# Optimization experiments

Hardware: AMD Instinct MI355X
Metric: run time of the kernel (lower is better)

## Reference

```python
import jax, jax.numpy as jnp
import numpy as np

B, C_IN, H, W = 8, 64, 224, 224
C_OUT, HID = 64, 64
KH = KW = 3
IN_SZ = C_IN * KH * KW  # 576, unfold feature size (c, kh, kw order)


def setup_inputs() -> dict:
    key = jax.random.key(0)
    k_x, k_w1, k_b1, k_w2, k_b2 = jax.random.split(key, 5)
    bound1 = 1.0 / np.sqrt(IN_SZ)
    bound2 = 1.0 / np.sqrt(HID)
    return {
        "x": jax.random.normal(k_x, (B, C_IN, H, W), dtype=jnp.float32),
        "W1": jax.random.uniform(k_w1, (HID, IN_SZ), jnp.float32, -bound1, bound1),
        "b1": jax.random.uniform(k_b1, (HID,), jnp.float32, -bound1, bound1),
        "W2": jax.random.uniform(k_w2, (C_OUT, HID), jnp.float32, -bound2, bound2),
        "b2": jax.random.uniform(k_b2, (C_OUT,), jnp.float32, -bound2, bound2),
    }


def reference(x, W1, b1, W2, b2):
    # First Linear over unfold patches == implicit-GEMM conv: W1 rows are
    # flattened (c, kh, kw) exactly matching F.unfold's feature ordering.
    w_conv = W1.reshape(HID, C_IN, KH, KW)
    h = jax.lax.conv_general_dilated(
        x, w_conv,
        window_strides=(1, 1),
        padding=((1, 1), (1, 1)),
        rhs_dilation=(1, 1),
        dimension_numbers=("NCHW", "OIHW", "NCHW"),
    ) + b1[None, :, None, None]
    h = jax.nn.relu(h)
    # Second Linear acts per patch location == pointwise (1x1) contraction.
    out = jnp.einsum("bchw,oc->bohw", h, W2) + b2[None, :, None, None]
    return out
```

## Files before the change

### kernel.cpp

```cpp
#include <hip/hip_runtime.h>

typedef __attribute__((ext_vector_type(8))) short bf16x8;
typedef __attribute__((ext_vector_type(4))) float f32x4;

static constexpr int HH = 224, WW = 224;
static constexpr int CIN = 64;

__device__ __forceinline__ ushort f2bf(float f) {
    unsigned u = __builtin_bit_cast(unsigned, f);
    u += 0x7FFFu + ((u >> 16) & 1u);
    return (ushort)(u >> 16);
}

__global__ void prep_kernel(const float* __restrict__ W1, const float* __restrict__ W2,
                            ushort* __restrict__ w1r, ushort* __restrict__ w2r) {
    const int idx = blockIdx.x * 256 + threadIdx.x;
    if (idx < 36864) {
        const int ch = idx >> 12;
        const int n = (idx >> 6) & 63;
        const int c = idx & 63;
        w1r[idx] = f2bf(W1[n * 576 + c * 9 + ch]);
    } else if (idx < 40960) {
        const int j = idx - 36864;
        w2r[j] = f2bf(W2[j]);
    }
}

__global__ __launch_bounds__(256, 3)
void mlpconv_kernel(const float* __restrict__ xin, const ushort* __restrict__ w1r,
                    const float* __restrict__ b1, const ushort* __restrict__ w2r,
                    const float* __restrict__ b2, float* __restrict__ out) {
    __shared__ ushort xs[10 * 40 * 64];

    const int tid = threadIdx.x;
    const int wave = tid >> 6;
    const int lane = tid & 63;
    const int l15 = lane & 15;
    const int quad = lane >> 4;

    const int x0 = blockIdx.x * 32;
    const int y0 = blockIdx.y * 8;
    const int b = blockIdx.z;

    const float* xg = xin + (size_t)b * (CIN * HH * WW);

    for (int e = tid; e < 6400; e += 256) {
        const int i = e % 10;
        const int t = e / 10;
        const int c = t & 63;
        const int r = t >> 6;
        const int gy = y0 + r - 1;
        const int gx4 = x0 - 4 + i * 4;
        float4 v = make_float4(0.f, 0.f, 0.f, 0.f);
        if (((unsigned)gy < (unsigned)HH) && ((unsigned)gx4 <= 220u))
            v = *reinterpret_cast<const float4*>(xg + (c * HH + gy) * WW + gx4);
        const int p0 = r * 40 + i * 4;
        xs[(p0 + 0) * 64 + (c ^ (((p0 + 0) & 7) * 8))] = f2bf(v.x);
        xs[(p0 + 1) * 64 + (c ^ (((p0 + 1) & 7) * 8))] = f2bf(v.y);
        xs[(p0 + 2) * 64 + (c ^ (((p0 + 2) & 7) * 8))] = f2bf(v.z);
        xs[(p0 + 3) * 64 + (c ^ (((p0 + 3) & 7) * 8))] = f2bf(v.w);
    }

    float b1v[4];
    #pragma unroll
    for (int nt = 0; nt < 4; ++nt) b1v[nt] = b1[nt * 16 + l15];

    f32x4 acc[4][4];
    #pragma unroll
    for (int mt = 0; mt < 4; ++mt)
        #pragma unroll
        for (int nt = 0; nt < 4; ++nt)
            acc[mt][nt] = (f32x4){b1v[nt], b1v[nt], b1v[nt], b1v[nt]};

    __syncthreads();

    #pragma unroll 2
    for (int ks = 0; ks < 18; ++ks) {
        const int ch = ks >> 1;
        const int s = ks & 1;
        const int dy = ch / 3, dx = ch - 3 * (ch / 3);
        const int ko = s * 32 + quad * 8;
        bf16x8 bfr[4];
        #pragma unroll
        for (int nt = 0; nt < 4; ++nt)
            bfr[nt] = *reinterpret_cast<const bf16x8*>(
                w1r + ch * 4096 + (nt * 16 + l15) * 64 + ko);
        const int kswz = ko ^ (((l15 + dx + 3) & 7) * 8);
        #pragma unroll
        for (int mt = 0; mt < 4; ++mt) {
            const int row = 2 * wave + (mt >> 1) + dy;
            const int col = (mt & 1) * 16 + l15 + dx + 3;
            const bf16x8 afr = *reinterpret_cast<const bf16x8*>(
                &xs[(row * 40 + col) * 64 + kswz]);
            #pragma unroll
            for (int nt = 0; nt < 4; ++nt)
                acc[mt][nt] = __builtin_amdgcn_mfma_f32_16x16x32_bf16(
                    afr, bfr[nt], acc[mt][nt], 0, 0, 0);
        }
    }

    __syncthreads();

    float4 b2q[4];
    #pragma unroll
    for (int it = 0; it < 4; ++it)
        b2q[it] = *reinterpret_cast<const float4*>(b2 + it * 16 + quad * 4);

    bf16x8 wa2[2][4];
    #pragma unroll
    for (int k2 = 0; k2 < 2; ++k2)
        #pragma unroll
        for (int it = 0; it < 4; ++it)
            wa2[k2][it] = *reinterpret_cast<const bf16x8*>(
                w2r + (it * 16 + l15) * 64 + k2 * 32 + quad * 8);

    ushort* myh = &xs[wave * (16 * 72)];
    float* outg = out + (size_t)b * (64 * HH * WW);

    #pragma unroll
    for (int mt = 0; mt < 4; ++mt) {
        #pragma unroll
        for (int ni = 0; ni < 4; ++ni)
            #pragma unroll
            for (int r = 0; r < 4; ++r) {
                float v = acc[mt][ni][r];
                v = v > 0.f ? v : 0.f;
                myh[(quad * 4 + r) * 72 + ni * 16 + l15] = f2bf(v);
            }
        f32x4 acc2[4];
        #pragma unroll
        for (int it = 0; it < 4; ++it)
            acc2[it] = (f32x4){b2q[it].x, b2q[it].y, b2q[it].z, b2q[it].w};
        #pragma unroll
        for (int k2 = 0; k2 < 2; ++k2) {
            const bf16x8 hb = *reinterpret_cast<const bf16x8*>(
                &myh[l15 * 72 + k2 * 32 + quad * 8]);
            #pragma unroll
            for (int it = 0; it < 4; ++it)
                acc2[it] = __builtin_amdgcn_mfma_f32_16x16x32_bf16(
                    wa2[k2][it], hb, acc2[it], 0, 0, 0);
        }
        const int gy = y0 + 2 * wave + (mt >> 1);
        const int gx = x0 + (mt & 1) * 16 + l15;
        #pragma unroll
        for (int it = 0; it < 4; ++it)
            #pragma unroll
            for (int r = 0; r < 4; ++r) {
                const int o = it * 16 + quad * 4 + r;
                outg[(o * HH + gy) * WW + gx] = acc2[it][r];
            }
    }
}

extern "C" void kernel_launch(void* const* d_in, const int* in_sizes, int n_in,
                              void* d_out, int out_size, void* d_ws, size_t ws_size,
                              hipStream_t stream) {
    const float* x  = (const float*)d_in[0];
    const float* W1 = (const float*)d_in[1];
    const float* b1 = (const float*)d_in[2];
    const float* W2 = (const float*)d_in[3];
    const float* b2 = (const float*)d_in[4];
    float* out = (float*)d_out;

    ushort* w1r = (ushort*)d_ws;
    ushort* w2r = w1r + 9 * 64 * 64;

    prep_kernel<<<160, 256, 0, stream>>>(W1, W2, w1r, w2r);
    dim3 grid(WW / 32, HH / 8, 8);
    mlpconv_kernel<<<grid, dim3(256), 0, stream>>>(x, w1r, b1, w2r, b2, out);
}
```

Measured before the change: 288.4 us.

## Pre-pack input to padded NHWC bf16 and read conv operands directly from global

Adds a pre-pass that converts x from NCHW fp32 into a zero-bordered NHWC bf16 buffer in workspace. The main kernel then loads MFMA A fragments straight from global or L2 instead of staging a haloed tile through shared memory, which drops the LDS fill, the swizzle and the barrier. This raises occupancy to 4 blocks per CU. The cost is an extra full read and write of the input (about 51 MB of bf16) plus two extra launches, and the path runs only when the workspace is large enough, otherwise it falls back to the old kernel.

```diff
diff --git a/kernel.cpp b/kernel.cpp
--- a/kernel.cpp
+++ b/kernel.cpp
@@ -4,7 +4,9 @@
 typedef __attribute__((ext_vector_type(4))) float f32x4;
 
 static constexpr int HH = 224, WW = 224;
-static constexpr int CIN = 64;
+static constexpr int HP = 226, WP = 226;
+static constexpr size_t XH_ELEMS = (size_t)8 * HP * WP * 64;
+static constexpr size_t WS_NEED = 2 * (XH_ELEMS + 9 * 64 * 64 + 64 * 64);
 
 __device__ __forceinline__ ushort f2bf(float f) {
     unsigned u = __builtin_bit_cast(unsigned, f);
@@ -12,13 +14,11 @@
     return (ushort)(u >> 16);
 }
 
-__global__ void prep_kernel(const float* __restrict__ W1, const float* __restrict__ W2,
-                            ushort* __restrict__ w1r, ushort* __restrict__ w2r) {
+__global__ void prep_w(const float* __restrict__ W1, const float* __restrict__ W2,
+                       ushort* __restrict__ w1r, ushort* __restrict__ w2r) {
     const int idx = blockIdx.x * 256 + threadIdx.x;
     if (idx < 36864) {
-        const int ch = idx >> 12;
-        const int n = (idx >> 6) & 63;
-        const int c = idx & 63;
+        const int ch = idx >> 12, n = (idx >> 6) & 63, c = idx & 63;
         w1r[idx] = f2bf(W1[n * 576 + c * 9 + ch]);
     } else if (idx < 40960) {
         const int j = idx - 36864;
@@ -26,58 +26,174 @@
     }
 }
 
+__global__ void prep_border(ushort* __restrict__ xh) {
+    const int t = blockIdx.x * 256 + threadIdx.x;
+    const int b = t / 7200, r = t - b * 7200;
+    const int slot = r >> 3, cg = r & 7;
+    int yp, p;
+    if (slot < 226)      { yp = 0;   p = slot; }
+    else if (slot < 452) { yp = 225; p = slot - 226; }
+    else if (slot < 676) { p = 0;    yp = slot - 452 + 1; }
+    else                 { p = 225;  yp = slot - 676 + 1; }
+    bf16x8 z = {0, 0, 0, 0, 0, 0, 0, 0};
+    *reinterpret_cast<bf16x8*>(xh + (((size_t)b * HP + yp) * WP + p) * 64 + cg * 8) = z;
+}
+
+__global__ __launch_bounds__(256)
+void prep_x(const float* __restrict__ x, ushort* __restrict__ xh) {
+    __shared__ ushort row[224 * 72];
+    const int gy = blockIdx.x, b = blockIdx.y;
+    const float* xg = x + ((size_t)b * 64 * HH + gy) * WW;
+    for (int e = threadIdx.x; e < 3584; e += 256) {
+        const int c = e & 63;
+        const int x4 = (e >> 6) * 4;
+        const float4 v = *reinterpret_cast<const float4*>(xg + (size_t)c * HH * WW + x4);
+        row[(x4 + 0) * 72 + c] = f2bf(v.x);
+        row[(x4 + 1) * 72 + c] = f2bf(v.y);
+        row[(x4 + 2) * 72 + c] = f2bf(v.z);
+        row[(x4 + 3) * 72 + c] = f2bf(v.w);
+    }
+    __syncthreads();
+    ushort* dst = xh + (((size_t)b * HP + gy + 1) * WP + 1) * 64;
+    for (int e = threadIdx.x; e < 1792; e += 256) {
+        const int p = e >> 3, cg = e & 7;
+        const bf16x8 v = *reinterpret_cast<const bf16x8*>(&row[p * 72 + cg * 8]);
+        *reinterpret_cast<bf16x8*>(dst + p * 64 + cg * 8) = v;
+    }
+}
+
+__global__ __launch_bounds__(256, 4)
+void mlpconv_main(const ushort* __restrict__ xh, const ushort* __restrict__ w1r,
+                  const float* __restrict__ b1, const ushort* __restrict__ w2r,
+                  const float* __restrict__ b2, float* __restrict__ out) {
+    __shared__ ushort hs[4 * 16 * 72];
+
+    const int tid = threadIdx.x;
+    const int wave = tid >> 6, lane = tid & 63, l15 = lane & 15, quad = lane >> 4;
+    const int x0 = blockIdx.x * 32, y0 = blockIdx.y * 8, b = blockIdx.z;
+    const int ko = quad * 8;
+
+    const ushort* a0 = xh + (((size_t)b * HP + y0 + 2 * wave) * WP + x0 + l15) * 64 + ko;
+    const ushort* w1b = w1r + l15 * 64 + ko;
+
+    float b1v[4];
+    #pragma unroll
+    for (int nt = 0; nt < 4; ++nt) b1v[nt] = b1[nt * 16 + l15];
+
+    f32x4 acc[4][4];
+    #pragma unroll
+    for (int mt = 0; mt < 4; ++mt)
+        #pragma unroll
+        for (int nt = 0; nt < 4; ++nt)
+            acc[mt][nt] = (f32x4){b1v[nt], b1v[nt], b1v[nt], b1v[nt]};
+
+    #pragma unroll
+    for (int ch = 0; ch < 9; ++ch) {
+        const int dy = ch / 3, dx = ch - 3 * (ch / 3);
+        #pragma unroll
+        for (int s = 0; s < 2; ++s) {
+            bf16x8 bfr[4];
+            #pragma unroll
+            for (int nt = 0; nt < 4; ++nt)
+                bfr[nt] = *reinterpret_cast<const bf16x8*>(
+                    w1b + ch * 4096 + nt * 1024 + s * 32);
+            #pragma unroll
+            for (int mt = 0; mt < 4; ++mt) {
+                const bf16x8 afr = *reinterpret_cast<const bf16x8*>(
+                    a0 + (((mt >> 1) + dy) * WP + (mt & 1) * 16 + dx) * 64 + s * 32);
+                #pragma unroll
+                for (int nt = 0; nt < 4; ++nt)
+                    acc[mt][nt] = __builtin_amdgcn_mfma_f32_16x16x32_bf16(
+                        afr, bfr[nt], acc[mt][nt], 0, 0, 0);
+            }
+        }
+    }
+
+    float4 b2q[4];
+    #pragma unroll
+    for (int it = 0; it < 4; ++it)
+        b2q[it] = *reinterpret_cast<const float4*>(b2 + it * 16 + quad * 4);
+
+    bf16x8 wa2[2][4];
+    #pragma unroll
+    for (int k2 = 0; k2 < 2; ++k2)
+        #pragma unroll
+        for (int it = 0; it < 4; ++it)
+            wa2[k2][it] = *reinterpret_cast<const bf16x8*>(
+                w2r + (it * 16 + l15) * 64 + k2 * 32 + quad * 8);
+
+    ushort* myh = &hs[wave * (16 * 72)];
+    float* outg = out + (size_t)b * (64 * HH * WW);
+
+    #pragma unroll
+    for (int mt = 0; mt < 4; ++mt) {
+        #pragma unroll
+        for (int ni = 0; ni < 4; ++ni)
+            #pragma unroll
+            for (int r = 0; r < 4; ++r) {
+                float v = acc[mt][ni][r];
+                v = v > 0.f ? v : 0.f;
+                myh[(quad * 4 + r) * 72 + ni * 16 + l15] = f2bf(v);
+            }
+        f32x4 acc2[4];
+        #pragma unroll
+        for (int it = 0; it < 4; ++it)
+            acc2[it] = (f32x4){b2q[it].x, b2q[it].y, b2q[it].z, b2q[it].w};
+        #pragma unroll
+        for (int k2 = 0; k2 < 2; ++k2) {
+            const bf16x8 hb = *reinterpret_cast<const bf16x8*>(
+                &myh[l15 * 72 + k2 * 32 + quad * 8]);
+            #pragma unroll
+            for (int it = 0; it < 4; ++it)
+                acc2[it] = __builtin_amdgcn_mfma_f32_16x16x32_bf16(
+                    wa2[k2][it], hb, acc2[it], 0, 0, 0);
+        }
+        const int gy = y0 + 2 * wave + (mt >> 1);
+        const int gx = x0 + (mt & 1) * 16 + l15;
+        #pragma unroll
+        for (int it = 0; it < 4; ++it)
+            #pragma unroll
+            for (int r = 0; r < 4; ++r) {
+                const int o = it * 16 + quad * 4 + r;
+                outg[(o * HH + gy) * WW + gx] = acc2[it][r];
+            }
+    }
+}
+
 __global__ __launch_bounds__(256, 3)
-void mlpconv_kernel(const float* __restrict__ xin, const ushort* __restrict__ w1r,
-                    const float* __restrict__ b1, const ushort* __restrict__ w2r,
-                    const float* __restrict__ b2, float* __restrict__ out) {
+void mlpconv_fallback(const float* __restrict__ xin, const ushort* __restrict__ w1r,
+                      const float* __restrict__ b1, const ushort* __restrict__ w2r,
+                      const float* __restrict__ b2, float* __restrict__ out) {
     __shared__ ushort xs[10 * 40 * 64];
-
     const int tid = threadIdx.x;
-    const int wave = tid >> 6;
-    const int lane = tid & 63;
-    const int l15 = lane & 15;
-    const int quad = lane >> 4;
-
-    const int x0 = blockIdx.x * 32;
-    const int y0 = blockIdx.y * 8;
-    const int b = blockIdx.z;
-
-    const float* xg = xin + (size_t)b * (CIN * HH * WW);
-
+    const int wave = tid >> 6, lane = tid & 63, l15 = lane & 15, quad = lane >> 4;
+    const int x0 = blockIdx.x * 32, y0 = blockIdx.y * 8, b = blockIdx.z;
+    const float* xg = xin + (size_t)b * (64 * HH * WW);
     for (int e = tid; e < 6400; e += 256) {
-        const int i = e % 10;
-        const int t = e / 10;
-        const int c = t & 63;
-        const int r = t >> 6;
-        const int gy = y0 + r - 1;
-        const int gx4 = x0 - 4 + i * 4;
+        const int i = e % 10, t = e / 10, c = t & 63, r = t >> 6;
+        const int gy = y0 + r - 1, gx4 = x0 - 4 + i * 4;
         float4 v = make_float4(0.f, 0.f, 0.f, 0.f);
         if (((unsigned)gy < (unsigned)HH) && ((unsigned)gx4 <= 220u))
-            v = *reinterpret_cast<const float4*>(xg + (c * HH + gy) * WW + gx4);
+            v = *reinterpret_cast<const float4*>(xg + ((size_t)c * HH + gy) * WW + gx4);
         const int p0 = r * 40 + i * 4;
         xs[(p0 + 0) * 64 + (c ^ (((p0 + 0) & 7) * 8))] = f2bf(v.x);
         xs[(p0 + 1) * 64 + (c ^ (((p0 + 1) & 7) * 8))] = f2bf(v.y);
         xs[(p0 + 2) * 64 + (c ^ (((p0 + 2) & 7) * 8))] = f2bf(v.z);
         xs[(p0 + 3) * 64 + (c ^ (((p0 + 3) & 7) * 8))] = f2bf(v.w);
     }
-
     float b1v[4];
     #pragma unroll
     for (int nt = 0; nt < 4; ++nt) b1v[nt] = b1[nt * 16 + l15];
-
     f32x4 acc[4][4];
     #pragma unroll
     for (int mt = 0; mt < 4; ++mt)
         #pragma unroll
         for (int nt = 0; nt < 4; ++nt)
             acc[mt][nt] = (f32x4){b1v[nt], b1v[nt], b1v[nt], b1v[nt]};
-
     __syncthreads();
-
     #pragma unroll 2
     for (int ks = 0; ks < 18; ++ks) {
-        const int ch = ks >> 1;
-        const int s = ks & 1;
+        const int ch = ks >> 1, s = ks & 1;
         const int dy = ch / 3, dx = ch - 3 * (ch / 3);
         const int ko = s * 32 + quad * 8;
         bf16x8 bfr[4];
@@ -98,14 +214,11 @@
                     afr, bfr[nt], acc[mt][nt], 0, 0, 0);
         }
     }
-
     __syncthreads();
-
     float4 b2q[4];
     #pragma unroll
     for (int it = 0; it < 4; ++it)
         b2q[it] = *reinterpret_cast<const float4*>(b2 + it * 16 + quad * 4);
-
     bf16x8 wa2[2][4];
     #pragma unroll
     for (int k2 = 0; k2 < 2; ++k2)
@@ -113,10 +226,8 @@
         for (int it = 0; it < 4; ++it)
             wa2[k2][it] = *reinterpret_cast<const bf16x8*>(
                 w2r + (it * 16 + l15) * 64 + k2 * 32 + quad * 8);
-
     ushort* myh = &xs[wave * (16 * 72)];
     float* outg = out + (size_t)b * (64 * HH * WW);
-
     #pragma unroll
     for (int mt = 0; mt < 4; ++mt) {
         #pragma unroll
@@ -162,10 +273,20 @@
     const float* b2 = (const float*)d_in[4];
     float* out = (float*)d_out;
 
-    ushort* w1r = (ushort*)d_ws;
-    ushort* w2r = w1r + 9 * 64 * 64;
-
-    prep_kernel<<<160, 256, 0, stream>>>(W1, W2, w1r, w2r);
-    dim3 grid(WW / 32, HH / 8, 8);
-    mlpconv_kernel<<<grid, dim3(256), 0, stream>>>(x, w1r, b1, w2r, b2, out);
-}
+    if (ws_size >= WS_NEED) {
+        ushort* xh  = (ushort*)d_ws;
+        ushort* w1r = xh + XH_ELEMS;
+        ushort* w2r = w1r + 9 * 64 * 64;
+        prep_w<<<160, 256, 0, stream>>>(W1, W2, w1r, w2r);
+        prep_border<<<225, 256, 0, stream>>>(xh);
+        prep_x<<<dim3(HH, 8), 256, 0, stream>>>(x, xh);
+        dim3 grid(WW / 32, HH / 8, 8);
+        mlpconv_main<<<grid, dim3(256), 0, stream>>>(xh, w1r, b1, w2r, b2, out);
+    } else {
+        ushort* w1r = (ushort*)d_ws;
+        ushort* w2r = w1r + 9 * 64 * 64;
+        prep_w<<<160, 256, 0, stream>>>(W1, W2, w1r, w2r);
+        dim3 grid(WW / 32, HH / 8, 8);
+        mlpconv_fallback<<<grid, dim3(256), 0, stream>>>(x, w1r, b1, w2r, b2, out);
+    }
+}
```

Result: slower. 364.3 us (+26.4%).
